# Optimization experiments

Measured on AMD Instinct MI355X. Metric: run time of the kernel, lower is better.

## Reference

```python
import jax, jax.numpy as jnp
import numpy as np

B, N, D = 4, 2048, 1024
H, DH = 16, 64
INNER = H * DH
FF = 4 * D
EPS = 1e-5


def _layernorm(x, g, b):
    mu = jnp.mean(x, axis=-1, keepdims=True)
    var = jnp.var(x, axis=-1, keepdims=True)
    return (x - mu) * jax.lax.rsqrt(var + EPS) * g + b


def setup_inputs() -> dict:
    key = jax.random.key(0)
    ks = jax.random.split(key, 16)
    s = lambda i, shape, scale: jax.random.normal(ks[i], shape, dtype=jnp.float32) * scale
    return {
        "x": s(0, (B, N, D), 1.0),
        "ln1_g": jnp.ones((D,), jnp.float32),
        "ln1_b": jnp.zeros((D,), jnp.float32),
        "w_qkv": s(1, (D, 3 * INNER), D ** -0.5),
        "w_out": s(2, (INNER, D), INNER ** -0.5),
        "b_out": jnp.zeros((D,), jnp.float32),
        "ln2_g": jnp.ones((D,), jnp.float32),
        "ln2_b": jnp.zeros((D,), jnp.float32),
        "w_ff1": s(3, (D, FF), D ** -0.5),
        "b_ff1": jnp.zeros((FF,), jnp.float32),
        "w_ff2": s(4, (FF, D), FF ** -0.5),
        "b_ff2": jnp.zeros((D,), jnp.float32),
        "w_halt": s(5, (D, 1), D ** -0.5),
        "b_halt": jnp.zeros((1,), jnp.float32),
    }


def reference(x, ln1_g, ln1_b, w_qkv, w_out, b_out, ln2_g, ln2_b,
              w_ff1, b_ff1, w_ff2, b_ff2, w_halt, b_halt):
    scale = DH ** -0.5
    # --- PreNorm attention ---
    h = _layernorm(x, ln1_g, ln1_b)
    qkv = h @ w_qkv                      # [B, N, 3*INNER]
    q, k, v = jnp.split(qkv, 3, axis=-1)
    split_heads = lambda t: t.reshape(B, N, H, DH).transpose(0, 2, 1, 3)  # b h n d
    q, k, v = map(split_heads, (q, k, v))
    sim = jnp.einsum('bhid,bhjd->bhij', q, k) * scale  # [B,H,N,N]
    causal_mask = jnp.triu(jnp.ones((N, N), bool), k=1)
    sim = jnp.where(causal_mask, -jnp.finfo(sim.dtype).max, sim)
    attn = jax.nn.softmax(sim, axis=-1)
    out = jnp.einsum('bhij,bhjd->bhid', attn, v)
    out = out.transpose(0, 2, 1, 3).reshape(B, N, INNER)
    x = out @ w_out + b_out + x
    # --- PreNorm feedforward ---
    h = _layernorm(x, ln2_g, ln2_b)
    h = jax.nn.gelu(h @ w_ff1 + b_ff1, approximate=False) @ w_ff2 + b_ff2
    x = h + x
    # --- halt logits ---
    halt = (jnp.mean(x, axis=1) @ w_halt + b_halt)[:, 0]  # [B]
    return x, halt
```

## Files before the change

kernel.cpp:

```cpp
#include <hip/hip_runtime.h>
#include <stdint.h>


typedef unsigned short u16;
typedef __attribute__((ext_vector_type(8))) short short8v;
typedef __attribute__((ext_vector_type(4))) float f32x4;
typedef __attribute__((ext_vector_type(4))) u16 u16x4;

#define B_ 4
#define N_ 2048
#define D_ 1024
#define H_ 16
#define DH_ 64
#define ROWS_ (B_ * N_)

__device__ __forceinline__ u16 f2bf(float f) {
  union { float f; unsigned u; } v; v.f = f;
  unsigned r = v.u + 0x7fffu + ((v.u >> 16) & 1u);
  return (u16)(r >> 16);
}

__device__ __forceinline__ f32x4 mfma_b(short8v a, short8v b, f32x4 c) {
  asm volatile("v_mfma_f32_16x16x32_bf16 %0, %1, %2, %0" : "+v"(c) : "v"(a), "v"(b));
  return c;
}
__device__ __forceinline__ f32x4 mfma_b_vc(short8v a, short8v b, f32x4 c) {
  asm volatile("s_nop 1\n\tv_mfma_f32_16x16x32_bf16 %0, %1, %2, %0" : "+v"(c) : "v"(a), "v"(b));
  return c;
}
__device__ __forceinline__ f32x4 accfence(f32x4 v) {
  asm volatile("s_nop 7" : "+v"(v));
  return v;
}

__device__ __forceinline__ void async16(const void* g, void* l) {
  __builtin_amdgcn_global_load_lds((__attribute__((address_space(1))) unsigned int*)g,
                                   (__attribute__((address_space(3))) unsigned int*)l,
                                   16, 0, 0);
}

#define SWZ8(row, chunk) ((((chunk) ^ ((row) & 7)) << 3))

__global__ __launch_bounds__(256) void ln_kernel(const float* __restrict__ x,
    const float* __restrict__ gam, const float* __restrict__ bet,
    u16* __restrict__ out) {
  const int row = blockIdx.x;
  const int t = threadIdx.x;
  const float4 v = ((const float4*)(x + (size_t)row * D_))[t];
  float s  = v.x + v.y + v.z + v.w;
  float ss = v.x*v.x + v.y*v.y + v.z*v.z + v.w*v.w;
#pragma unroll
  for (int o = 32; o >= 1; o >>= 1) { s += __shfl_xor(s, o); ss += __shfl_xor(ss, o); }
  __shared__ float red[8];
  const int w = t >> 6;
  if ((t & 63) == 0) { red[w] = s; red[4 + w] = ss; }
  __syncthreads();
  s  = red[0] + red[1] + red[2] + red[3];
  ss = red[4] + red[5] + red[6] + red[7];
  const float mean = s * (1.0f / D_);
  const float var  = ss * (1.0f / D_) - mean * mean;
  const float rstd = rsqrtf(var + 1e-5f);
  const float4 g4 = ((const float4*)gam)[t];
  const float4 b4 = ((const float4*)bet)[t];
  u16x4 o4;
  o4.x = f2bf((v.x - mean) * rstd * g4.x + b4.x);
  o4.y = f2bf((v.y - mean) * rstd * g4.y + b4.y);
  o4.z = f2bf((v.z - mean) * rstd * g4.z + b4.z);
  o4.w = f2bf((v.w - mean) * rstd * g4.w + b4.w);
  *(u16x4*)(out + (size_t)row * D_ + t * 4) = o4;
}

__global__ __launch_bounds__(256) void transpose_all(
    const float* __restrict__ wqkv, const float* __restrict__ wout,
    const float* __restrict__ wff1, const float* __restrict__ wff2,
    u16* __restrict__ wqkvT, u16* __restrict__ woutT,
    u16* __restrict__ wff1T, u16* __restrict__ wff2T) {
  __shared__ float tile[32][33];
  int id = blockIdx.x;
  const float* W; u16* WT; int K, N, nt, kt;
  if (id < 3072)      { W = wqkv; WT = wqkvT; K = 1024; N = 3072; nt = id % 96;  kt = id / 96; }
  else if (id < 4096) { id -= 3072; W = wout; WT = woutT; K = 1024; N = 1024; nt = id % 32;  kt = id / 32; }
  else if (id < 8192) { id -= 4096; W = wff1; WT = wff1T; K = 1024; N = 4096; nt = id % 128; kt = id / 128; }
  else                { id -= 8192; W = wff2; WT = wff2T; K = 4096; N = 1024; nt = id % 32;  kt = id / 32; }
  const int n0 = nt * 32, k0 = kt * 32;
  const int tx = threadIdx.x, ty = threadIdx.y;
#pragma unroll
  for (int i = 0; i < 4; ++i)
    tile[ty + i * 8][tx] = W[(size_t)(k0 + ty + i * 8) * N + n0 + tx];
  __syncthreads();
#pragma unroll
  for (int i = 0; i < 4; ++i)
    WT[(size_t)(n0 + ty + i * 8) * K + k0 + tx] = f2bf(tile[tx][ty + i * 8]);
}

__global__ __launch_bounds__(256) void transpose_v(const u16* __restrict__ qkv,
    u16* __restrict__ vt) {
  __shared__ u16 tile[32][33];
  const int bh = blockIdx.z;
  const int bb = bh >> 4, hh = bh & 15;
  const int n0 = blockIdx.x * 32, d0 = blockIdx.y * 32;
  const int tx = threadIdx.x, ty = threadIdx.y;
#pragma unroll
  for (int i = 0; i < 4; ++i)
    tile[ty + i * 8][tx] =
        qkv[(size_t)(bb * N_ + n0 + ty + i * 8) * 3072 + 2048 + hh * DH_ + d0 + tx];
  __syncthreads();
#pragma unroll
  for (int i = 0; i < 4; ++i)
    vt[((size_t)bh * DH_ + d0 + ty + i * 8) * N_ + n0 + tx] = tile[tx][ty + i * 8];
}

template <int BK>
__global__ __launch_bounds__(256) void gemm_bt(
    const u16* __restrict__ A, const u16* __restrict__ BT,
    int N, int K, int mode, int gx, int rw,
    const float* __restrict__ bias, const float* __restrict__ res,
    float* __restrict__ outf, u16* __restrict__ outb) {
  constexpr int ROWB = BK * 2;
  constexpr int CH   = BK / 8;
  __shared__ alignas(16) u16 As[128 * BK];
  __shared__ alignas(16) u16 Bs[128 * BK];
  const int t = threadIdx.x;
  const int lane = t & 63, w = t >> 6;
  const int wm = w >> 1, wn = w & 1;
  const int cc = lane & 15, quad = lane >> 4;

  const int i   = blockIdx.x;
  const int xcd = i & 7;
  const int s   = i >> 3;
  const int rcols = gx / rw;
  const int rh  = (gridDim.x >> 3) / rw;
  const int rcol = xcd % rcols, rrow = xcd / rcols;
  const int lx = s % rw, ly = s / rw;
  const int n0 = (rcol * rw + lx) * 128;
  const int m0 = (rrow * rh + ly) * 128;

  const f32x4 fz = {0.f, 0.f, 0.f, 0.f};
  f32x4 acc[4][4];
#pragma unroll
  for (int i2 = 0; i2 < 4; ++i2)
#pragma unroll
    for (int j = 0; j < 4; ++j) acc[i2][j] = fz;

  const int off0 = t * 16;
  for (int k0 = 0; k0 < K; k0 += BK) {
#pragma unroll
    for (int r = 0; r < BK / 16; ++r) {
      const int off = r * 4096 + off0;
      const int row = off / ROWB;
      const int cl  = ((off >> 4) & (CH - 1)) ^ (row & (CH - 1));
      async16(A  + (size_t)(m0 + row) * K + k0 + cl * 8, (char*)As + off);
      async16(BT + (size_t)(n0 + row) * K + k0 + cl * 8, (char*)Bs + off);
    }
    __syncthreads();
#pragma unroll
    for (int kk = 0; kk < BK / 32; ++kk) {
      short8v a[4], b[4];
#pragma unroll
      for (int i2 = 0; i2 < 4; ++i2)
        a[i2] = *(const short8v*)(As + (wm * 64 + i2 * 16 + cc) * BK +
                                  (((kk * 4 + quad) ^ (cc & (CH - 1))) << 3));
#pragma unroll
      for (int j = 0; j < 4; ++j)
        b[j] = *(const short8v*)(Bs + (wn * 64 + j * 16 + cc) * BK +
                                 (((kk * 4 + quad) ^ (cc & (CH - 1))) << 3));
#pragma unroll
      for (int i2 = 0; i2 < 4; ++i2)
#pragma unroll
        for (int j = 0; j < 4; ++j) acc[i2][j] = mfma_b(a[i2], b[j], acc[i2][j]);
    }
    __syncthreads();
  }

#pragma unroll
  for (int i2 = 0; i2 < 4; ++i2) {
    const int row = m0 + wm * 64 + i2 * 16 + quad * 4;
#pragma unroll
    for (int j = 0; j < 4; ++j) {
      const int col = n0 + wn * 64 + j * 16 + cc;
      f32x4 v = accfence(acc[i2][j]);
#pragma unroll
      for (int r = 0; r < 4; ++r) {
        const size_t idx = (size_t)(row + r) * N + col;
        float val = v[r];
        if (mode == 0) {
          outb[idx] = f2bf(val);
        } else if (mode == 2) {
          val += bias[col];
          const float zz = val * fmaf(val * val, 0.044715f, 1.0f);
          const float e = __builtin_amdgcn_exp2f(-2.3022082f * zz);
          val = val * __builtin_amdgcn_rcpf(1.0f + e);
          outb[idx] = f2bf(val);
        } else {
          outf[idx] = val + bias[col] + res[idx];
        }
      }
    }
  }
}

__global__ __launch_bounds__(256, 2) void attn_kernel(const u16* __restrict__ qkv,
    const u16* __restrict__ vt, u16* __restrict__ outp) {
  const int f  = blockIdx.x;
  const int p  = (f >> 3) & 7;
  const int g  = ((f >> 6) << 3) | (f & 7);
  const int hh = g & 15, bb = g >> 4;
  const int t = threadIdx.x, lane = t & 63, w = t >> 6;
  const int cc = lane & 15, quad = lane >> 4;

  __shared__ alignas(16) u16 Ks[2][64 * 64];
  __shared__ alignas(16) u16 Vs[2][64 * 64];
  __shared__ alignas(16) u16 Ps[4][16 * 64];

  const u16* kbase = qkv + (size_t)bb * N_ * 3072 + 1024 + hh * DH_;
  const u16* vbase = vt + ((size_t)(bb * H_ + hh)) * DH_ * N_;

  const int soff0 = t * 16;
#pragma unroll
  for (int r = 0; r < 2; ++r) {
    const int off = r * 4096 + soff0;
    const int row = off >> 7;
    const int cl  = ((off >> 4) & 7) ^ (row & 7);
    async16(kbase + (size_t)row * 3072 + cl * 8, (char*)Ks[0] + off);
    async16(vbase + (size_t)row * N_ + cl * 8,   (char*)Vs[0] + off);
  }

  const f32x4 fz = {0.f, 0.f, 0.f, 0.f};
  const float C1 = 0.18033688011112042f;
  const float C2 = -11.541560327111707f;

  int bufc = 0;
#pragma unroll
  for (int ci = 0; ci < 2; ++ci) {
    const int qc = ci ? 15 - p : p;
    const int q0 = qc * 128;
    const int ktmax = 2 * qc + 1;

    short8v qa[2][2];
#pragma unroll
    for (int s = 0; s < 2; ++s)
#pragma unroll
      for (int h = 0; h < 2; ++h)
        qa[s][h] = *(const short8v*)(qkv +
            (size_t)(bb * N_ + q0 + s * 64 + w * 16 + cc) * 3072 +
            hh * DH_ + h * 32 + quad * 8);

    f32x4 of[2][4];
    float rs[2][4];
#pragma unroll
    for (int s = 0; s < 2; ++s)
#pragma unroll
      for (int n = 0; n < 4; ++n) { of[s][n] = fz; rs[s][n] = 0.f; }

    for (int kt = 0; kt <= ktmax; ++kt) {
      const int k0 = kt * 64;
      const int cur = bufc & 1;
      __syncthreads();

      if ((kt < ktmax) | (ci == 0)) {
        const int k1 = (kt < ktmax) ? k0 + 64 : 0;
#pragma unroll
        for (int r = 0; r < 2; ++r) {
          const int off = r * 4096 + soff0;
          const int row = off >> 7;
          const int cl  = ((off >> 4) & 7) ^ (row & 7);
          async16(kbase + (size_t)(k1 + row) * 3072 + cl * 8, (char*)Ks[cur ^ 1] + off);
          async16(vbase + (size_t)row * N_ + k1 + cl * 8,     (char*)Vs[cur ^ 1] + off);
        }
      }

      const u16* KsB = Ks[cur];
      const u16* VsB = Vs[cur];
      short8v kb[4][2], vb[4][2];
#pragma unroll
      for (int j = 0; j < 4; ++j)
#pragma unroll
        for (int h = 0; h < 2; ++h) {
          kb[j][h] = *(const short8v*)(KsB + (j * 16 + cc) * 64 + SWZ8(cc, h * 4 + quad));
          vb[j][h] = *(const short8v*)(VsB + (j * 16 + cc) * 64 + SWZ8(cc, h * 4 + quad));
        }

#pragma unroll
      for (int s = 0; s < 2; ++s) {
        const int Rbase = q0 + s * 64 + w * 16;
        if (k0 > Rbase + 15) continue;

        f32x4 sr[4];
#pragma unroll
        for (int j = 0; j < 4; ++j) {
          f32x4 z = fz;
          z = mfma_b_vc(qa[s][0], kb[j][0], z);
          z = mfma_b(qa[s][1], kb[j][1], z);
          sr[j] = accfence(z);
        }

        if (k0 + 63 > Rbase) {
#pragma unroll
          for (int j = 0; j < 4; ++j) {
            const int kcol = k0 + j * 16 + cc;
#pragma unroll
            for (int r = 0; r < 4; ++r) {
              float pv = __builtin_amdgcn_exp2f(fmaf(sr[j][r], C1, C2));
              pv = (kcol <= Rbase + quad * 4 + r) ? pv : 0.f;
              sr[j][r] = pv;
              rs[s][r] += pv;
            }
          }
        } else {
#pragma unroll
          for (int j = 0; j < 4; ++j)
#pragma unroll
            for (int r = 0; r < 4; ++r) {
              const float pv = __builtin_amdgcn_exp2f(fmaf(sr[j][r], C1, C2));
              sr[j][r] = pv;
              rs[s][r] += pv;
            }
        }

#pragma unroll
        for (int j = 0; j < 4; ++j)
#pragma unroll
          for (int r = 0; r < 4; ++r) {
            union { float f; unsigned u; } cv; cv.f = sr[j][r];
            const int rho = quad * 4 + r;
            const int Lc  = j * 2 + (cc >> 3);
            Ps[w][rho * 64 + (((Lc ^ (rho & 7)) << 3) | (cc & 7))] =
                (u16)((cv.u + 0x8000u) >> 16);
          }
        const short8v pa0 = *(const short8v*)(&Ps[w][cc * 64 + SWZ8(cc, quad)]);
        const short8v pa1 = *(const short8v*)(&Ps[w][cc * 64 + SWZ8(cc, 4 + quad)]);
#pragma unroll
        for (int n = 0; n < 4; ++n) {
          of[s][n] = mfma_b(pa0, vb[n][0], of[s][n]);
          of[s][n] = mfma_b(pa1, vb[n][1], of[s][n]);
        }
      }
      ++bufc;
    }

#pragma unroll
    for (int o = 1; o < 16; o <<= 1)
#pragma unroll
      for (int s = 0; s < 2; ++s)
#pragma unroll
        for (int r = 0; r < 4; ++r) rs[s][r] += __shfl_xor(rs[s][r], o);

#pragma unroll
    for (int s = 0; s < 2; ++s) {
      float inv[4];
#pragma unroll
      for (int r = 0; r < 4; ++r) inv[r] = 1.0f / rs[s][r];
#pragma unroll
      for (int n = 0; n < 4; ++n) {
        f32x4 o = accfence(of[s][n]);
#pragma unroll
        for (int r = 0; r < 4; ++r) {
          const size_t row = (size_t)(bb * N_ + q0 + s * 64 + w * 16 + quad * 4 + r);
          outp[row * 1024 + hh * DH_ + n * 16 + cc] = f2bf(o[r] * inv[r]);
        }
      }
    }
  }
}

__global__ void halt_init(float* __restrict__ hout, const float* __restrict__ bh) {
  if (threadIdx.x < B_) hout[threadIdx.x] = bh[0];
}

__global__ __launch_bounds__(256) void halt_partial(const float* __restrict__ xf,
    const float* __restrict__ wh, float* __restrict__ hout) {
  const int bb = blockIdx.y, sl = blockIdx.x;
  const size_t base = ((size_t)bb * N_ + sl * 64) * D_;
  float p = 0.f;
  for (int e = threadIdx.x; e < 64 * D_; e += 256)
    p += xf[base + e] * wh[e & (D_ - 1)];
#pragma unroll
  for (int o = 32; o >= 1; o >>= 1) p += __shfl_xor(p, o);
  __shared__ float red[4];
  const int w = threadIdx.x >> 6;
  if ((threadIdx.x & 63) == 0) red[w] = p;
  __syncthreads();
  if (threadIdx.x == 0)
    atomicAdd(&hout[bb], (red[0] + red[1] + red[2] + red[3]) * (1.0f / N_));
}

extern "C" void kernel_launch(void* const* d_in, const int* in_sizes, int n_in,
                              void* d_out, int out_size, void* d_ws, size_t ws_size,
                              hipStream_t stream) {
  (void)in_sizes; (void)n_in; (void)out_size; (void)ws_size;
  const float* x      = (const float*)d_in[0];
  const float* ln1_g  = (const float*)d_in[1];
  const float* ln1_b  = (const float*)d_in[2];
  const float* w_qkv  = (const float*)d_in[3];
  const float* w_out  = (const float*)d_in[4];
  const float* b_out  = (const float*)d_in[5];
  const float* ln2_g  = (const float*)d_in[6];
  const float* ln2_b  = (const float*)d_in[7];
  const float* w_ff1  = (const float*)d_in[8];
  const float* b_ff1  = (const float*)d_in[9];
  const float* w_ff2  = (const float*)d_in[10];
  const float* b_ff2  = (const float*)d_in[11];
  const float* w_halt = (const float*)d_in[12];
  const float* b_halt = (const float*)d_in[13];

  float* out_x    = (float*)d_out;
  float* out_halt = out_x + (size_t)ROWS_ * D_;

  char* ws = (char*)d_ws;
  u16* wqkvT = (u16*)(ws + 0);
  u16* woutT = (u16*)(ws + 6291456);
  u16* wff1T = (u16*)(ws + 8388608);
  u16* wff2T = (u16*)(ws + 16777216);
  char* RB   = ws + 25165824;
  u16* qkvb  = (u16*)(RB);
  u16* h1    = (u16*)(RB + 50331648);
  u16* attno = h1;
  u16* vtb   = (u16*)(RB + 67108864);
  u16* h2    = (u16*)(RB);
  u16* ff1b  = (u16*)(RB + 16777216);

  const dim3 tb(32, 8);
  transpose_all<<<12288, tb, 0, stream>>>(w_qkv, w_out, w_ff1, w_ff2,
                                          wqkvT, woutT, wff1T, wff2T);
  ln_kernel<<<ROWS_, 256, 0, stream>>>(x, ln1_g, ln1_b, h1);
  gemm_bt<64><<<1536, 256, 0, stream>>>(h1, wqkvT, 3072, 1024, 0, 24, 12,
                                        nullptr, nullptr, nullptr, qkvb);
  transpose_v<<<dim3(64, 2, 64), tb, 0, stream>>>(qkvb, vtb);
  attn_kernel<<<dim3(512), 256, 0, stream>>>(qkvb, vtb, attno);
  gemm_bt<128><<<512, 256, 0, stream>>>(attno, woutT, 1024, 1024, 1, 8, 8,
                                        b_out, x, out_x, nullptr);
  ln_kernel<<<ROWS_, 256, 0, stream>>>(out_x, ln2_g, ln2_b, h2);
  gemm_bt<64><<<2048, 256, 0, stream>>>(h2, wff1T, 4096, 1024, 2, 32, 16,
                                        b_ff1, nullptr, nullptr, ff1b);
  gemm_bt<128><<<512, 256, 0, stream>>>(ff1b, wff2T, 1024, 4096, 3, 8, 8,
                                        b_ff2, out_x, out_x, nullptr);
  halt_init<<<1, 64, 0, stream>>>(out_halt, b_halt);
  halt_partial<<<dim3(32, 4), 256, 0, stream>>>(out_x, w_halt, out_halt);
}
```

Measured before the change: 577.2 us.

## Add 256x256-tile 512-thread GEMM for QKV and FF1 projections

Introduces a new bf16 MFMA GEMM kernel with 256x256 output tiles, 8 waves, double-buffered async LDS loads, and loads for the next k-tile spread across four compute phases. It replaces the 128x128 kernel for the QKV and FF1 projections, including the fused bias+GELU epilogue, to raise arithmetic intensity and overlap memory with compute. The output projection also switches from BK=128 to BK=64. The larger tiles use 128KB of LDS and many accumulator registers, which limits occupancy to one block per CU, and the grid becomes coarser (384/512 blocks).

New measurement: 649.3 us. +12.5%, slower.

```diff
diff --git a/kernel.cpp b/kernel.cpp
--- a/kernel.cpp
+++ b/kernel.cpp
@@ -110,6 +110,120 @@
     vt[((size_t)bh * DH_ + d0 + ty + i * 8) * N_ + n0 + tx] = tile[tx][ty + i * 8];
 }
 
+__global__ __launch_bounds__(512) void gemm256(
+    const u16* __restrict__ A, const u16* __restrict__ BT,
+    int N, int K, int mode, int gx, int rw,
+    const float* __restrict__ bias, u16* __restrict__ outb) {
+  __shared__ alignas(16) u16 As[2][2][128 * 64];
+  __shared__ alignas(16) u16 Bs[2][2][128 * 64];
+  const int t = threadIdx.x;
+  const int lane = t & 63, w = t >> 6;
+  const int wm = w >> 2, wn = w & 3;
+  const int cc = lane & 15, quad = lane >> 4;
+  const int hb = wn >> 1, lb = (wn & 1) * 64;
+
+  const int i   = blockIdx.x;
+  const int xcd = i & 7;
+  const int s   = i >> 3;
+  const int rcols = gx / rw;
+  const int rh  = (gridDim.x >> 3) / rw;
+  const int rcol = xcd % rcols, rrow = xcd / rcols;
+  const int lx = s % rw, ly = s / rw;
+  const int n0 = (rcol * rw + lx) * 256;
+  const int m0 = (rrow * rh + ly) * 256;
+
+  const f32x4 fz = {0.f, 0.f, 0.f, 0.f};
+  f32x4 acc[8][4];
+#pragma unroll
+  for (int i2 = 0; i2 < 8; ++i2)
+#pragma unroll
+    for (int j = 0; j < 4; ++j) acc[i2][j] = fz;
+
+  const int t16 = t * 16;
+#pragma unroll
+  for (int h = 0; h < 2; ++h)
+#pragma unroll
+    for (int pass = 0; pass < 2; ++pass) {
+      const int off = pass * 8192 + t16;
+      const int row = off >> 7;
+      const int cl  = ((off >> 4) & 7) ^ (row & 7);
+      async16(A  + (size_t)(m0 + h * 128 + row) * K + cl * 8,
+              (char*)&As[0][h][0] + off);
+      async16(BT + (size_t)(n0 + h * 128 + row) * K + cl * 8,
+              (char*)&Bs[0][h][0] + off);
+    }
+
+  const int NT = K >> 6;
+  for (int kt = 0; kt < NT; ++kt) {
+    const int cur = kt & 1, nxt = cur ^ 1;
+    const bool more = (kt + 1 < NT);
+    const int k1 = (kt + 1) << 6;
+#pragma unroll
+    for (int ph = 0; ph < 4; ++ph) {
+      __builtin_amdgcn_s_barrier();
+      if (ph == 0) __builtin_amdgcn_sched_barrier(0);
+      if (more) {
+#pragma unroll
+        for (int pass = 0; pass < 2; ++pass) {
+          const int off = pass * 8192 + t16;
+          const int row = off >> 7;
+          const int cl  = ((off >> 4) & 7) ^ (row & 7);
+          if (ph < 2)
+            async16(A + (size_t)(m0 + ph * 128 + row) * K + k1 + cl * 8,
+                    (char*)&As[nxt][ph][0] + off);
+          else
+            async16(BT + (size_t)(n0 + (ph - 2) * 128 + row) * K + k1 + cl * 8,
+                    (char*)&Bs[nxt][ph - 2][0] + off);
+        }
+      }
+      if (ph == 0) {
+        if (more) asm volatile("s_waitcnt vmcnt(2)" ::: "memory");
+        else      asm volatile("s_waitcnt vmcnt(0)" ::: "memory");
+        __builtin_amdgcn_sched_barrier(0);
+      }
+      const int kk = ph >> 1, rh2 = ph & 1;
+      short8v a[4], b[4];
+#pragma unroll
+      for (int i2 = 0; i2 < 4; ++i2)
+        a[i2] = *(const short8v*)(&As[cur][wm][((rh2 * 4 + i2) * 16 + cc) * 64 +
+                                               SWZ8(cc, kk * 4 + quad)]);
+#pragma unroll
+      for (int j = 0; j < 4; ++j)
+        b[j] = *(const short8v*)(&Bs[cur][hb][(lb + j * 16 + cc) * 64 +
+                                              SWZ8(cc, kk * 4 + quad)]);
+      __builtin_amdgcn_s_setprio(1);
+#pragma unroll
+      for (int i2 = 0; i2 < 4; ++i2)
+#pragma unroll
+        for (int j = 0; j < 4; ++j)
+          acc[rh2 * 4 + i2][j] = mfma_b(a[i2], b[j], acc[rh2 * 4 + i2][j]);
+      __builtin_amdgcn_s_setprio(0);
+    }
+  }
+
+#pragma unroll
+  for (int i2 = 0; i2 < 8; ++i2) {
+    const int row = m0 + wm * 128 + i2 * 16 + quad * 4;
+#pragma unroll
+    for (int j = 0; j < 4; ++j) {
+      const int col = n0 + wn * 64 + j * 16 + cc;
+      f32x4 v = accfence(acc[i2][j]);
+#pragma unroll
+      for (int r = 0; r < 4; ++r) {
+        const size_t idx = (size_t)(row + r) * N + col;
+        float val = v[r];
+        if (mode == 2) {
+          val += bias[col];
+          const float zz = val * fmaf(val * val, 0.044715f, 1.0f);
+          const float e = __builtin_amdgcn_exp2f(-2.3022082f * zz);
+          val = val * __builtin_amdgcn_rcpf(1.0f + e);
+        }
+        outb[idx] = f2bf(val);
+      }
+    }
+  }
+}
+
 template <int BK>
 __global__ __launch_bounds__(256) void gemm_bt(
     const u16* __restrict__ A, const u16* __restrict__ BT,
@@ -423,15 +537,15 @@
   transpose_all<<<12288, tb, 0, stream>>>(w_qkv, w_out, w_ff1, w_ff2,
                                           wqkvT, woutT, wff1T, wff2T);
   ln_kernel<<<ROWS_, 256, 0, stream>>>(x, ln1_g, ln1_b, h1);
-  gemm_bt<64><<<1536, 256, 0, stream>>>(h1, wqkvT, 3072, 1024, 0, 24, 12,
-                                        nullptr, nullptr, nullptr, qkvb);
+  gemm256<<<384, 512, 0, stream>>>(h1, wqkvT, 3072, 1024, 0, 12, 6,
+                                   nullptr, qkvb);
   transpose_v<<<dim3(64, 2, 64), tb, 0, stream>>>(qkvb, vtb);
   attn_kernel<<<dim3(512), 256, 0, stream>>>(qkvb, vtb, attno);
-  gemm_bt<128><<<512, 256, 0, stream>>>(attno, woutT, 1024, 1024, 1, 8, 8,
-                                        b_out, x, out_x, nullptr);
+  gemm_bt<64><<<512, 256, 0, stream>>>(attno, woutT, 1024, 1024, 1, 8, 8,
+                                       b_out, x, out_x, nullptr);
   ln_kernel<<<ROWS_, 256, 0, stream>>>(out_x, ln2_g, ln2_b, h2);
-  gemm_bt<64><<<2048, 256, 0, stream>>>(h2, wff1T, 4096, 1024, 2, 32, 16,
-                                        b_ff1, nullptr, nullptr, ff1b);
+  gemm256<<<512, 512, 0, stream>>>(h2, wff1T, 4096, 1024, 2, 16, 8,
+                                   b_ff1, ff1b);
   gemm_bt<128><<<512, 256, 0, stream>>>(ff1b, wff2T, 1024, 4096, 3, 8, 8,
                                         b_ff2, out_x, out_x, nullptr);
   halt_init<<<1, 64, 0, stream>>>(out_halt, b_halt);
```
